# Performance work log

Hardware: AMD Instinct MI355X
Metric: run time of the kernel (lower is better)

The kernel has to match this reference:

```python
import jax, jax.numpy as jnp
import numpy as np

B, T, ENC, DEC, U = 64, 2048, 512, 512, 128

def setup_inputs() -> dict:
    key = jax.random.key(0)
    ks = jax.random.split(key, 8)
    s_dec = 1.0 / np.sqrt(DEC)
    s_enc = 1.0 / np.sqrt(ENC)
    s_u = 1.0 / np.sqrt(U)
    return {
        "decoder_hidden": jax.random.normal(ks[0], (B, DEC), jnp.float32),
        "encoder_outputs": jax.random.normal(ks[1], (B, T, ENC), jnp.float32),
        "Wa": jax.random.normal(ks[2], (DEC, U), jnp.float32) * s_dec,
        "ba": jnp.zeros((U,), jnp.float32),
        "Wb": jax.random.normal(ks[3], (ENC, U), jnp.float32) * s_enc,
        "bb": jnp.zeros((U,), jnp.float32),
        "Wv": jax.random.normal(ks[4], (U, 1), jnp.float32) * s_u,
        "bv": jnp.zeros((1,), jnp.float32),
    }

def reference(decoder_hidden, encoder_outputs, Wa, ba, Wb, bb, Wv, bv):
    # q: [B, 1, U] — decoder hidden projected, broadcast over time
    q = (decoder_hidden @ Wa + ba)[:, None, :]
    # k: [B, T, U]
    k = jnp.einsum('bte,eu->btu', encoder_outputs, Wb) + bb
    # score: [B, T, 1]
    score = jnp.tanh(q + k) @ Wv + bv
    attn = jax.nn.softmax(score, axis=1)          # [B, T, 1]
    context = jnp.sum(attn * encoder_outputs, axis=1)  # [B, ENC]
    return context, attn
```

## Files before the change

kernel.cpp:

```cpp
#include <hip/hip_runtime.h>
#include <math.h>

#define B_   64
#define T_   2048
#define ENC_ 512
#define U_   128

typedef __attribute__((ext_vector_type(8))) short short8;
typedef __attribute__((ext_vector_type(4))) float float4v;

__device__ inline unsigned short bf16_rtn(float x) {
    unsigned u = __float_as_uint(x);
    unsigned r = u + 0x7FFFu + ((u >> 16) & 1u);
    return (unsigned short)(r >> 16);
}
__device__ inline float bf16_to_f32(unsigned short h) {
    return __uint_as_float(((unsigned)h) << 16);
}

__global__ void qproj_kernel(const float* __restrict__ dh,
                             const float* __restrict__ Wa,
                             const float* __restrict__ ba,
                             const float* __restrict__ bb,
                             float* __restrict__ q) {
    const int b = blockIdx.x;
    const int u = threadIdx.x;
    const float* dhb = dh + b * ENC_;
    float acc = 0.f;
#pragma unroll 8
    for (int e = 0; e < ENC_; ++e)
        acc += dhb[e] * Wa[e * U_ + u];
    q[b * U_ + u] = acc + ba[u] + bb[u];
}

__global__ void wprep_kernel(const float* __restrict__ Wb,
                             unsigned short* __restrict__ whi,
                             unsigned short* __restrict__ wlo) {
    const int fid = blockIdx.x;
    const int c   = fid >> 3;
    const int gn  = fid & 7;
    const int L   = threadIdx.x;
    const int n   = gn * 16 + (L & 15);
    const int k0  = c * 32 + (L >> 4) * 8;
    short8 hi, lo;
#pragma unroll
    for (int j = 0; j < 8; ++j) {
        const float x = Wb[(size_t)(k0 + j) * U_ + n];
        const unsigned short h = bf16_rtn(x);
        hi[j] = (short)h;
        lo[j] = (short)bf16_rtn(x - bf16_to_f32(h));
    }
    *(short8*)(whi + ((size_t)fid * 64 + L) * 8) = hi;
    *(short8*)(wlo + ((size_t)fid * 64 + L) * 8) = lo;
}

#define MBLK 64

__global__ __launch_bounds__(256)
void score_mfma_kernel(const float* __restrict__ enc,
                       const unsigned short* __restrict__ whi,
                       const unsigned short* __restrict__ wlo,
                       const float* __restrict__ q,
                       const float* __restrict__ Wv,
                       float* __restrict__ scores) {
    __shared__ __align__(16) short Ahi[2][64 * 32];
    __shared__ __align__(16) short Alo[2][64 * 32];

    const int tid = threadIdx.x;
    const int w   = tid >> 6;
    const int L   = tid & 63;
    const int m0  = blockIdx.x * MBLK;
    const int b   = m0 >> 11;

    const int srow  = tid >> 2;
    const int sqd   = tid & 3;
    const int sfrag = ((srow >> 4) * 4 + sqd) * 16 + (srow & 15);
    const float* encRow = enc + (size_t)(m0 + srow) * ENC_ + sqd * 8;

    float4v acc[8];
#pragma unroll
    for (int gn = 0; gn < 8; ++gn) acc[gn] = (float4v)0.f;

    {
        const float4 a0 = *(const float4*)(encRow);
        const float4 a1 = *(const float4*)(encRow + 4);
        const float xs[8] = {a0.x, a0.y, a0.z, a0.w, a1.x, a1.y, a1.z, a1.w};
        short8 h, l;
#pragma unroll
        for (int j = 0; j < 8; ++j) {
            const unsigned short hb = bf16_rtn(xs[j]);
            h[j] = (short)hb;
            l[j] = (short)bf16_rtn(xs[j] - bf16_to_f32(hb));
        }
        *(short8*)(&Ahi[0][sfrag * 8]) = h;
        *(short8*)(&Alo[0][sfrag * 8]) = l;
    }
    __syncthreads();

    for (int c = 0; c < 16; ++c) {
        const int cur = c & 1;
        float4 n0, n1;
        if (c < 15) {
            n0 = *(const float4*)(encRow + (c + 1) * 32);
            n1 = *(const float4*)(encRow + (c + 1) * 32 + 4);
        }
        const short8 ah = *(const short8*)(&Ahi[cur][(w * 64 + L) * 8]);
        const short8 al = *(const short8*)(&Alo[cur][(w * 64 + L) * 8]);
        const unsigned short* bh_base = whi + ((size_t)(c * 8) * 64 + L) * 8;
        const unsigned short* bl_base = wlo + ((size_t)(c * 8) * 64 + L) * 8;
#pragma unroll
        for (int gn = 0; gn < 8; ++gn) {
            const short8 bh = *(const short8*)(bh_base + (size_t)gn * 64 * 8);
            const short8 bl = *(const short8*)(bl_base + (size_t)gn * 64 * 8);
            acc[gn] = __builtin_amdgcn_mfma_f32_16x16x32_bf16(ah, bh, acc[gn], 0, 0, 0);
            acc[gn] = __builtin_amdgcn_mfma_f32_16x16x32_bf16(ah, bl, acc[gn], 0, 0, 0);
            acc[gn] = __builtin_amdgcn_mfma_f32_16x16x32_bf16(al, bh, acc[gn], 0, 0, 0);
        }
        if (c < 15) {
            const int nxt = cur ^ 1;
            const float xs[8] = {n0.x, n0.y, n0.z, n0.w, n1.x, n1.y, n1.z, n1.w};
            short8 h, l;
#pragma unroll
            for (int j = 0; j < 8; ++j) {
                const unsigned short hb = bf16_rtn(xs[j]);
                h[j] = (short)hb;
                l[j] = (short)bf16_rtn(xs[j] - bf16_to_f32(hb));
            }
            *(short8*)(&Ahi[nxt][sfrag * 8]) = h;
            *(short8*)(&Alo[nxt][sfrag * 8]) = l;
        }
        __syncthreads();
    }

    const int n15 = L & 15;
    float qv[8], wvv[8];
#pragma unroll
    for (int gn = 0; gn < 8; ++gn) {
        qv[gn]  = q[b * U_ + gn * 16 + n15];
        wvv[gn] = Wv[gn * 16 + n15];
    }
    const int rbase = m0 + w * 16 + (L >> 4) * 4;
#pragma unroll
    for (int r = 0; r < 4; ++r) {
        float s = 0.f;
#pragma unroll
        for (int gn = 0; gn < 8; ++gn)
            s += tanhf(qv[gn] + acc[gn][r]) * wvv[gn];
        s += __shfl_xor(s, 1, 64);
        s += __shfl_xor(s, 2, 64);
        s += __shfl_xor(s, 4, 64);
        s += __shfl_xor(s, 8, 64);
        if (n15 == 0) scores[rbase + r] = s;
    }
}

__global__ void softmax_kernel(const float* __restrict__ scores,
                               float* __restrict__ attn) {
    const int b   = blockIdx.x;
    const int tid = threadIdx.x;
    const float* s = scores + b * T_;

    float v[8];
    float mx = -1e30f;
#pragma unroll
    for (int i = 0; i < 8; ++i) {
        v[i] = s[tid + i * 256];
        mx = fmaxf(mx, v[i]);
    }
    for (int off = 1; off < 64; off <<= 1)
        mx = fmaxf(mx, __shfl_xor(mx, off, 64));
    __shared__ float redm[4];
    __shared__ float reds[4];
    if ((tid & 63) == 0) redm[tid >> 6] = mx;
    __syncthreads();
    mx = fmaxf(fmaxf(redm[0], redm[1]), fmaxf(redm[2], redm[3]));

    float sum = 0.f;
#pragma unroll
    for (int i = 0; i < 8; ++i) {
        v[i] = expf(v[i] - mx);
        sum += v[i];
    }
    for (int off = 1; off < 64; off <<= 1)
        sum += __shfl_xor(sum, off, 64);
    if ((tid & 63) == 0) reds[tid >> 6] = sum;
    __syncthreads();
    sum = reds[0] + reds[1] + reds[2] + reds[3];
    const float inv = 1.f / sum;
#pragma unroll
    for (int i = 0; i < 8; ++i)
        attn[b * T_ + tid + i * 256] = v[i] * inv;
}

__global__ void zero_ctx_kernel(float* __restrict__ ctx) {
    ctx[blockIdx.x * 256 + threadIdx.x] = 0.f;
}

__global__ __launch_bounds__(256)
void context_atomic_kernel(const float* __restrict__ enc,
                           const float* __restrict__ attn,
                           float* __restrict__ ctx) {
    const int ch  = blockIdx.x;
    const int b   = blockIdx.y;
    const int tid = threadIdx.x;

    __shared__ float aw[128];
    if (tid < 128) aw[tid] = attn[b * T_ + ch * 128 + tid];
    __syncthreads();

    const float* ebase = enc + ((size_t)b * T_ + ch * 128) * ENC_;
    float sx = 0.f, sy = 0.f;
#pragma unroll 4
    for (int t = 0; t < 128; ++t) {
        const float wgt = aw[t];
        const float2 v = *(const float2*)(ebase + (size_t)t * ENC_ + tid * 2);
        sx += wgt * v.x;
        sy += wgt * v.y;
    }
    atomicAdd(&ctx[b * ENC_ + tid * 2], sx);
    atomicAdd(&ctx[b * ENC_ + tid * 2 + 1], sy);
}

extern "C" void kernel_launch(void* const* d_in, const int* in_sizes, int n_in,
                              void* d_out, int out_size, void* d_ws, size_t ws_size,
                              hipStream_t stream) {
    const float* dh  = (const float*)d_in[0];
    const float* enc = (const float*)d_in[1];
    const float* Wa  = (const float*)d_in[2];
    const float* ba  = (const float*)d_in[3];
    const float* Wb  = (const float*)d_in[4];
    const float* bb  = (const float*)d_in[5];
    const float* Wv  = (const float*)d_in[6];

    float* out      = (float*)d_out;
    float* ctx      = out;
    float* attn_out = out + (B_ * ENC_);

    float* ws           = (float*)d_ws;
    float* q            = ws;
    float* scores       = ws + 8192;
    unsigned short* whi = (unsigned short*)(ws + 8192 + B_ * T_);
    unsigned short* wlo = whi + 16 * 8 * 64 * 8;

    qproj_kernel<<<B_, U_, 0, stream>>>(dh, Wa, ba, bb, q);
    wprep_kernel<<<128, 64, 0, stream>>>(Wb, whi, wlo);
    score_mfma_kernel<<<(B_ * T_) / MBLK, 256, 0, stream>>>(enc, whi, wlo, q, Wv, scores);
    softmax_kernel<<<B_, 256, 0, stream>>>(scores, attn_out);
    zero_ctx_kernel<<<(B_ * ENC_) / 256, 256, 0, stream>>>(ctx);
    context_atomic_kernel<<<dim3(16, B_), 256, 0, stream>>>(enc, attn_out, ctx);
}
```

Baseline: 507.1 us.

## Fuse score, softmax and context into one kernel with unnormalized exp weights

The score kernel now computes exp(score) without max subtraction, and in the same block accumulates the weighted encoder rows into an unnormalized context and a per-batch partition sum with atomics. A small normalize kernel then divides both the context and the attention weights by that sum. This removes the separate softmax pass and the second full read of the encoder tensor from a cold kernel, since the block rereads rows it just loaded, which may still be cached. The tile grows to 128 rows per block with two accumulator sets, tanh uses an exp-based approximation, and the low-part bf16 split truncates instead of rounding. Skipping the max subtraction risks overflow for large scores.

After: 498.1 us. No clear change (-1.8%).

```diff
diff --git a/kernel.cpp b/kernel.cpp
--- a/kernel.cpp
+++ b/kernel.cpp
@@ -5,6 +5,7 @@
 #define T_   2048
 #define ENC_ 512
 #define U_   128
+#define NC   16
 
 typedef __attribute__((ext_vector_type(8))) short short8;
 typedef __attribute__((ext_vector_type(4))) float float4v;
@@ -16,6 +17,25 @@
 }
 __device__ inline float bf16_to_f32(unsigned short h) {
     return __uint_as_float(((unsigned)h) << 16);
+}
+
+__device__ inline void cvt_split8(const float4 a0, const float4 a1,
+                                  short8& h, short8& l) {
+    const float xs[8] = {a0.x, a0.y, a0.z, a0.w, a1.x, a1.y, a1.z, a1.w};
+#pragma unroll
+    for (int j = 0; j < 8; ++j) {
+        const unsigned u  = __float_as_uint(xs[j]);
+        const unsigned r  = u + 0x7FFFu + ((u >> 16) & 1u);
+        const unsigned hb = r >> 16;
+        h[j] = (short)hb;
+        const float d = xs[j] - __uint_as_float(hb << 16);
+        l[j] = (short)(__float_as_uint(d) >> 16);
+    }
+}
+
+__device__ inline float fast_tanh(float x) {
+    const float e = __expf(2.0f * x);
+    return 1.0f - 2.0f / (e + 1.0f);
 }
 
 __global__ void qproj_kernel(const float* __restrict__ dh,
@@ -26,11 +46,15 @@
     const int b = blockIdx.x;
     const int u = threadIdx.x;
     const float* dhb = dh + b * ENC_;
-    float acc = 0.f;
-#pragma unroll 8
-    for (int e = 0; e < ENC_; ++e)
-        acc += dhb[e] * Wa[e * U_ + u];
-    q[b * U_ + u] = acc + ba[u] + bb[u];
+    float a0 = 0.f, a1 = 0.f, a2 = 0.f, a3 = 0.f;
+#pragma unroll 4
+    for (int e = 0; e < ENC_; e += 4) {
+        a0 += dhb[e + 0] * Wa[(e + 0) * U_ + u];
+        a1 += dhb[e + 1] * Wa[(e + 1) * U_ + u];
+        a2 += dhb[e + 2] * Wa[(e + 2) * U_ + u];
+        a3 += dhb[e + 3] * Wa[(e + 3) * U_ + u];
+    }
+    q[b * U_ + u] = ((a0 + a1) + (a2 + a3)) + ba[u] + bb[u];
 }
 
 __global__ void wprep_kernel(const float* __restrict__ Wb,
@@ -54,17 +78,25 @@
     *(short8*)(wlo + ((size_t)fid * 64 + L) * 8) = lo;
 }
 
-#define MBLK 64
-
-__global__ __launch_bounds__(256)
-void score_mfma_kernel(const float* __restrict__ enc,
-                       const unsigned short* __restrict__ whi,
-                       const unsigned short* __restrict__ wlo,
-                       const float* __restrict__ q,
-                       const float* __restrict__ Wv,
-                       float* __restrict__ scores) {
-    __shared__ __align__(16) short Ahi[2][64 * 32];
-    __shared__ __align__(16) short Alo[2][64 * 32];
+__global__ void zero_kernel(float* __restrict__ p, int n) {
+    const int i = blockIdx.x * 256 + threadIdx.x;
+    if (i < n) p[i] = 0.f;
+}
+
+#define MBLK 128
+
+__global__ __launch_bounds__(256, 2)
+void score_ctx_kernel(const float* __restrict__ enc,
+                      const unsigned short* __restrict__ whi,
+                      const unsigned short* __restrict__ wlo,
+                      const float* __restrict__ q,
+                      const float* __restrict__ Wv,
+                      float* __restrict__ expw,
+                      float* __restrict__ uctx,
+                      float* __restrict__ Zsum) {
+    __shared__ __align__(16) short Ahi[2][4096];
+    __shared__ __align__(16) short Alo[2][4096];
+    __shared__ float ew[MBLK];
 
     const int tid = threadIdx.x;
     const int w   = tid >> 6;
@@ -72,62 +104,63 @@
     const int m0  = blockIdx.x * MBLK;
     const int b   = m0 >> 11;
 
-    const int srow  = tid >> 2;
-    const int sqd   = tid & 3;
-    const int sfrag = ((srow >> 4) * 4 + sqd) * 16 + (srow & 15);
-    const float* encRow = enc + (size_t)(m0 + srow) * ENC_ + sqd * 8;
-
-    float4v acc[8];
-#pragma unroll
-    for (int gn = 0; gn < 8; ++gn) acc[gn] = (float4v)0.f;
+    const int srow = tid >> 2;
+    const int sqd  = tid & 3;
+    const int sf0  = ((srow >> 4) * 4 + sqd) * 16 + (srow & 15);
+    const int sf1  = (((srow >> 4) + 4) * 4 + sqd) * 16 + (srow & 15);
+    const float* encR0 = enc + (size_t)(m0 + srow) * ENC_ + sqd * 8;
+    const float* encR1 = encR0 + (size_t)64 * ENC_;
+
+    float4v acc0[8], acc1[8];
+#pragma unroll
+    for (int gn = 0; gn < 8; ++gn) { acc0[gn] = (float4v)0.f; acc1[gn] = (float4v)0.f; }
 
     {
-        const float4 a0 = *(const float4*)(encRow);
-        const float4 a1 = *(const float4*)(encRow + 4);
-        const float xs[8] = {a0.x, a0.y, a0.z, a0.w, a1.x, a1.y, a1.z, a1.w};
         short8 h, l;
-#pragma unroll
-        for (int j = 0; j < 8; ++j) {
-            const unsigned short hb = bf16_rtn(xs[j]);
-            h[j] = (short)hb;
-            l[j] = (short)bf16_rtn(xs[j] - bf16_to_f32(hb));
-        }
-        *(short8*)(&Ahi[0][sfrag * 8]) = h;
-        *(short8*)(&Alo[0][sfrag * 8]) = l;
+        cvt_split8(*(const float4*)(encR0), *(const float4*)(encR0 + 4), h, l);
+        *(short8*)(&Ahi[0][sf0 * 8]) = h;
+        *(short8*)(&Alo[0][sf0 * 8]) = l;
+        cvt_split8(*(const float4*)(encR1), *(const float4*)(encR1 + 4), h, l);
+        *(short8*)(&Ahi[0][sf1 * 8]) = h;
+        *(short8*)(&Alo[0][sf1 * 8]) = l;
     }
     __syncthreads();
 
-    for (int c = 0; c < 16; ++c) {
+    for (int c = 0; c < NC; ++c) {
         const int cur = c & 1;
-        float4 n0, n1;
-        if (c < 15) {
-            n0 = *(const float4*)(encRow + (c + 1) * 32);
-            n1 = *(const float4*)(encRow + (c + 1) * 32 + 4);
-        }
-        const short8 ah = *(const short8*)(&Ahi[cur][(w * 64 + L) * 8]);
-        const short8 al = *(const short8*)(&Alo[cur][(w * 64 + L) * 8]);
+        float4 p00, p01, p10, p11;
+        if (c < NC - 1) {
+            p00 = *(const float4*)(encR0 + (c + 1) * 32);
+            p01 = *(const float4*)(encR0 + (c + 1) * 32 + 4);
+            p10 = *(const float4*)(encR1 + (c + 1) * 32);
+            p11 = *(const float4*)(encR1 + (c + 1) * 32 + 4);
+        }
+        const short8 ah0 = *(const short8*)(&Ahi[cur][((2 * w + 0) * 64 + L) * 8]);
+        const short8 al0 = *(const short8*)(&Alo[cur][((2 * w + 0) * 64 + L) * 8]);
+        const short8 ah1 = *(const short8*)(&Ahi[cur][((2 * w + 1) * 64 + L) * 8]);
+        const short8 al1 = *(const short8*)(&Alo[cur][((2 * w + 1) * 64 + L) * 8]);
         const unsigned short* bh_base = whi + ((size_t)(c * 8) * 64 + L) * 8;
         const unsigned short* bl_base = wlo + ((size_t)(c * 8) * 64 + L) * 8;
 #pragma unroll
         for (int gn = 0; gn < 8; ++gn) {
-            const short8 bh = *(const short8*)(bh_base + (size_t)gn * 64 * 8);
-            const short8 bl = *(const short8*)(bl_base + (size_t)gn * 64 * 8);
-            acc[gn] = __builtin_amdgcn_mfma_f32_16x16x32_bf16(ah, bh, acc[gn], 0, 0, 0);
-            acc[gn] = __builtin_amdgcn_mfma_f32_16x16x32_bf16(ah, bl, acc[gn], 0, 0, 0);
-            acc[gn] = __builtin_amdgcn_mfma_f32_16x16x32_bf16(al, bh, acc[gn], 0, 0, 0);
-        }
-        if (c < 15) {
+            const short8 bh = *(const short8*)(bh_base + (size_t)gn * 512);
+            const short8 bl = *(const short8*)(bl_base + (size_t)gn * 512);
+            acc0[gn] = __builtin_amdgcn_mfma_f32_16x16x32_bf16(ah0, bh, acc0[gn], 0, 0, 0);
+            acc0[gn] = __builtin_amdgcn_mfma_f32_16x16x32_bf16(ah0, bl, acc0[gn], 0, 0, 0);
+            acc0[gn] = __builtin_amdgcn_mfma_f32_16x16x32_bf16(al0, bh, acc0[gn], 0, 0, 0);
+            acc1[gn] = __builtin_amdgcn_mfma_f32_16x16x32_bf16(ah1, bh, acc1[gn], 0, 0, 0);
+            acc1[gn] = __builtin_amdgcn_mfma_f32_16x16x32_bf16(ah1, bl, acc1[gn], 0, 0, 0);
+            acc1[gn] = __builtin_amdgcn_mfma_f32_16x16x32_bf16(al1, bh, acc1[gn], 0, 0, 0);
+        }
+        if (c < NC - 1) {
             const int nxt = cur ^ 1;
-            const float xs[8] = {n0.x, n0.y, n0.z, n0.w, n1.x, n1.y, n1.z, n1.w};
             short8 h, l;
-#pragma unroll
-            for (int j = 0; j < 8; ++j) {
-                const unsigned short hb = bf16_rtn(xs[j]);
-                h[j] = (short)hb;
-                l[j] = (short)bf16_rtn(xs[j] - bf16_to_f32(hb));
-            }
-            *(short8*)(&Ahi[nxt][sfrag * 8]) = h;
-            *(short8*)(&Alo[nxt][sfrag * 8]) = l;
+            cvt_split8(p00, p01, h, l);
+            *(short8*)(&Ahi[nxt][sf0 * 8]) = h;
+            *(short8*)(&Alo[nxt][sf0 * 8]) = l;
+            cvt_split8(p10, p11, h, l);
+            *(short8*)(&Ahi[nxt][sf1 * 8]) = h;
+            *(short8*)(&Alo[nxt][sf1 * 8]) = l;
         }
         __syncthreads();
     }
@@ -139,86 +172,66 @@
         qv[gn]  = q[b * U_ + gn * 16 + n15];
         wvv[gn] = Wv[gn * 16 + n15];
     }
-    const int rbase = m0 + w * 16 + (L >> 4) * 4;
-#pragma unroll
-    for (int r = 0; r < 4; ++r) {
-        float s = 0.f;
-#pragma unroll
-        for (int gn = 0; gn < 8; ++gn)
-            s += tanhf(qv[gn] + acc[gn][r]) * wvv[gn];
-        s += __shfl_xor(s, 1, 64);
-        s += __shfl_xor(s, 2, 64);
-        s += __shfl_xor(s, 4, 64);
-        s += __shfl_xor(s, 8, 64);
-        if (n15 == 0) scores[rbase + r] = s;
-    }
-}
-
-__global__ void softmax_kernel(const float* __restrict__ scores,
-                               float* __restrict__ attn) {
-    const int b   = blockIdx.x;
-    const int tid = threadIdx.x;
-    const float* s = scores + b * T_;
-
-    float v[8];
-    float mx = -1e30f;
-#pragma unroll
-    for (int i = 0; i < 8; ++i) {
-        v[i] = s[tid + i * 256];
-        mx = fmaxf(mx, v[i]);
-    }
-    for (int off = 1; off < 64; off <<= 1)
-        mx = fmaxf(mx, __shfl_xor(mx, off, 64));
-    __shared__ float redm[4];
-    __shared__ float reds[4];
-    if ((tid & 63) == 0) redm[tid >> 6] = mx;
+#pragma unroll
+    for (int tt = 0; tt < 2; ++tt) {
+        const float4v* accp = tt ? acc1 : acc0;
+#pragma unroll
+        for (int r = 0; r < 4; ++r) {
+            float s = 0.f;
+#pragma unroll
+            for (int gn = 0; gn < 8; ++gn)
+                s += fast_tanh(qv[gn] + accp[gn][r]) * wvv[gn];
+            s += __shfl_xor(s, 1, 64);
+            s += __shfl_xor(s, 2, 64);
+            s += __shfl_xor(s, 4, 64);
+            s += __shfl_xor(s, 8, 64);
+            if (n15 == 0) {
+                const int rloc = (2 * w + tt) * 16 + (L >> 4) * 4 + r;
+                const float e = __expf(s);
+                ew[rloc] = e;
+                expw[m0 + rloc] = e;
+            }
+        }
+    }
     __syncthreads();
-    mx = fmaxf(fmaxf(redm[0], redm[1]), fmaxf(redm[2], redm[3]));
-
-    float sum = 0.f;
-#pragma unroll
-    for (int i = 0; i < 8; ++i) {
-        v[i] = expf(v[i] - mx);
-        sum += v[i];
-    }
-    for (int off = 1; off < 64; off <<= 1)
-        sum += __shfl_xor(sum, off, 64);
-    if ((tid & 63) == 0) reds[tid >> 6] = sum;
-    __syncthreads();
-    sum = reds[0] + reds[1] + reds[2] + reds[3];
-    const float inv = 1.f / sum;
-#pragma unroll
-    for (int i = 0; i < 8; ++i)
-        attn[b * T_ + tid + i * 256] = v[i] * inv;
-}
-
-__global__ void zero_ctx_kernel(float* __restrict__ ctx) {
-    ctx[blockIdx.x * 256 + threadIdx.x] = 0.f;
-}
-
-__global__ __launch_bounds__(256)
-void context_atomic_kernel(const float* __restrict__ enc,
-                           const float* __restrict__ attn,
-                           float* __restrict__ ctx) {
-    const int ch  = blockIdx.x;
-    const int b   = blockIdx.y;
-    const int tid = threadIdx.x;
-
-    __shared__ float aw[128];
-    if (tid < 128) aw[tid] = attn[b * T_ + ch * 128 + tid];
-    __syncthreads();
-
-    const float* ebase = enc + ((size_t)b * T_ + ch * 128) * ENC_;
+
+    const int col = tid * 2;
+    const float* ebase = enc + (size_t)m0 * ENC_ + col;
     float sx = 0.f, sy = 0.f;
-#pragma unroll 4
-    for (int t = 0; t < 128; ++t) {
-        const float wgt = aw[t];
-        const float2 v = *(const float2*)(ebase + (size_t)t * ENC_ + tid * 2);
+#pragma unroll 8
+    for (int t = 0; t < MBLK; ++t) {
+        const float wgt = ew[t];
+        const float2 v = *(const float2*)(ebase + (size_t)t * ENC_);
         sx += wgt * v.x;
         sy += wgt * v.y;
     }
-    atomicAdd(&ctx[b * ENC_ + tid * 2], sx);
-    atomicAdd(&ctx[b * ENC_ + tid * 2 + 1], sy);
+    atomicAdd(&uctx[b * ENC_ + col], sx);
+    atomicAdd(&uctx[b * ENC_ + col + 1], sy);
+
+    if (tid < 64) {
+        float z = ew[tid] + ew[tid + 64];
+        z += __shfl_xor(z, 1, 64);
+        z += __shfl_xor(z, 2, 64);
+        z += __shfl_xor(z, 4, 64);
+        z += __shfl_xor(z, 8, 64);
+        z += __shfl_xor(z, 16, 64);
+        z += __shfl_xor(z, 32, 64);
+        if (tid == 0) atomicAdd(&Zsum[b], z);
+    }
+}
+
+__global__ void normalize_kernel(const float* __restrict__ uctx,
+                                 const float* __restrict__ Zsum,
+                                 const float* __restrict__ expw,
+                                 float* __restrict__ ctx,
+                                 float* __restrict__ attn) {
+    const int idx = blockIdx.x * 256 + threadIdx.x;
+    if (idx < B_ * ENC_) {
+        ctx[idx] = uctx[idx] / Zsum[idx >> 9];
+    } else {
+        const int i2 = idx - B_ * ENC_;
+        attn[i2] = expw[i2] / Zsum[i2 >> 11];
+    }
 }
 
 extern "C" void kernel_launch(void* const* d_in, const int* in_sizes, int n_in,
@@ -236,16 +249,19 @@
     float* ctx      = out;
     float* attn_out = out + (B_ * ENC_);
 
-    float* ws           = (float*)d_ws;
-    float* q            = ws;
-    float* scores       = ws + 8192;
-    unsigned short* whi = (unsigned short*)(ws + 8192 + B_ * T_);
-    unsigned short* wlo = whi + 16 * 8 * 64 * 8;
+    float* ws   = (float*)d_ws;
+    float* q    = ws;
+    float* expw = ws + 8192;
+    float* uctx = ws + 8192 + B_ * T_;
+    float* Zs   = uctx + B_ * ENC_;
+    unsigned short* whi = (unsigned short*)(Zs + 64);
+    unsigned short* wlo = whi + 65536;
 
     qproj_kernel<<<B_, U_, 0, stream>>>(dh, Wa, ba, bb, q);
     wprep_kernel<<<128, 64, 0, stream>>>(Wb, whi, wlo);
-    score_mfma_kernel<<<(B_ * T_) / MBLK, 256, 0, stream>>>(enc, whi, wlo, q, Wv, scores);
-    softmax_kernel<<<B_, 256, 0, stream>>>(scores, attn_out);
-    zero_ctx_kernel<<<(B_ * ENC_) / 256, 256, 0, stream>>>(ctx);
-    context_atomic_kernel<<<dim3(16, B_), 256, 0, stream>>>(enc, attn_out, ctx);
-}
+    zero_kernel<<<129, 256, 0, stream>>>(uctx, B_ * ENC_ + B_);
+    score_ctx_kernel<<<(B_ * T_) / MBLK, 256, 0, stream>>>(enc, whi, wlo, q, Wv,
+                                                           expw, uctx, Zs);
+    normalize_kernel<<<(B_ * (ENC_ + T_)) / 256, 256, 0, stream>>>(uctx, Zs, expw,
+                                                                   ctx, attn_out);
+}
```
